# Performance work log

Measured on AMD Instinct MI355X. Metric: run time of the kernel, lower is better.

## Reference

```python
import jax, jax.numpy as jnp
import numpy as np

# dims: B batch, T timesteps, V nodes, D in-features, C channels, d pos-emb dim,
# TS = t_size (spatio-temporal window), P prediction steps, L layers (=4, fixed by GLU(C*4))
B, T, V, D, C, d, TS, P, L = 4, 12, 512, 1, 64, 8, 3, 12, 4
BETA = TS - 1


def setup_inputs() -> dict:
    key = jax.random.key(0)
    ks = jax.random.split(key, 30)
    n = lambda i, shape, s=1.0: jax.random.normal(ks[i], shape, dtype=jnp.float32) * s
    return dict(
        x=n(0, (B, T, V, D)),
        sape=n(1, (V, d)),
        tape=n(2, (B, T, 1, d)),
        srpe=n(3, (V, V, d)),
        trpe=n(4, (TS, 1, d)),
        zeros_x=jnp.zeros((B, BETA, V, C), jnp.float32),
        zeros_tape=jnp.zeros((B, BETA, 1, d), jnp.float32),
        range_mask=(jax.random.uniform(ks[5], (B, V, TS * V)) < 0.5).astype(jnp.float32),
        Wi=n(6, (D, C), D ** -0.5), bi=n(7, (C,), 0.02),
        gc_mu=n(8, (L, 6, d)), gc_sig=n(9, (L, 6, d), 0.5),
        Wg=n(10, (L, C, 2 * C), C ** -0.5), bg=n(11, (L, 2 * C), 0.02),
        Wsp=n(12, (L, d, 2 * C), d ** -0.5), Wtp=n(13, (L, d, 2 * C), d ** -0.5),
        fs_w=n(14, (L, C, C, T), (C * T) ** -0.5), fs_b=n(15, (L, C), 0.02),
        glu1_w=n(16, (L, 2 * C, C), C ** -0.5), glu1_b=n(17, (L, 2 * C), 0.02),
        gout_w=n(18, (8 * C, 4 * C), (4 * C) ** -0.5), gout_b=n(19, (8 * C,), 0.02),
        out_w=n(20, (P, 4 * C), (4 * C) ** -0.5), out_b=n(21, (P,), 0.02),
    )


def _glu_cv(w, b, y):
    # 1x1-conv GLU over channel dim of y: (B, Cin, V) -> (B, Cin, V)
    z = jnp.einsum('oc,bcv->bov', w, y) + b[None, :, None]
    zl, zr = jnp.split(z, 2, axis=1)
    return zl * jax.nn.sigmoid(zr)


def _forward(x, sape, tape, srpe, trpe, Wi, bi, gc_mu, gc_sig, Wg, bg, Wsp, Wtp,
             fs_w, fs_b, glu1_w, glu1_b, gout_w, gout_b, out_w, out_b,
             zeros_x, zeros_tape, range_mask):
    b_, t_ = x.shape[0], x.shape[1]
    v_ = sape.shape[0]
    ts = trpe.shape[0]
    widx = jnp.arange(t_)[:, None] + jnp.arange(ts)  # (T, t_size) sliding-window indices
    h = x @ Wi + bi                                   # InputLayer: B,T,V,C
    tape_pad = jnp.concatenate([zeros_tape, tape], axis=1)  # B,T+beta,1,d
    skips = []
    for l in range(gc_mu.shape[0]):
        mu, sig = gc_mu[l], gc_sig[l]
        gc = lambda emb, i: jnp.sum(-0.5 * (emb - mu[i]) ** 2 * sig[i] ** 2, axis=-1)
        # STPRI: Gaussian position-aware relation inference
        base = gc(sape, 0)[:, None] + gc(sape, 1)[None, :] + gc(srpe, 4)        # (V_i, V_j)
        per_t = gc(tape, 2)[:, :, 0][:, :, None] \
              + gc(tape_pad, 3)[:, :, 0][:, widx] \
              + gc(trpe, 5)[:, 0]                                               # B,T,t_size
        S = jnp.exp(per_t[:, :, :, None, None] + base)                          # B,T,k,i,j (<=1, safe)
        S = S.transpose(0, 1, 4, 2, 3).reshape(b_, t_, v_, ts * v_)             # B,T,j,(k*V+i)
        S = S * range_mask[:, None]                                             # masked relations
        # STPGConv: masked graph conv over the t_size*V window + gating
        x_pad = jnp.concatenate([zeros_x, h], axis=1)                           # B,T+beta,V,C
        xw = x_pad[:, widx].reshape(b_, t_, ts * v_, -1)                        # B,T,t_size*V,C
        g = jnp.einsum('btjm,btmc->btjc', S, xw) @ Wg[l] + bg[l]                # B,T,V,2C
        g = g + sape @ Wsp[l] + tape @ Wtp[l]                                   # +SE(V,2C) +TE(B,T,1,2C)
        gl, gr = jnp.split(g, 2, axis=-1)
        h = gl * jax.nn.sigmoid(gr)                                             # B,T,V,C
        # GFS: conv over time (kernel (1,T)) + GLU -> B,C,V
        y = jnp.einsum('bcvt,oct->bov', h.transpose(0, 3, 2, 1), fs_w[l]) + fs_b[l][None, :, None]
        skips.append(_glu_cv(glu1_w[l], glu1_b[l], y))
    s = _glu_cv(gout_w, gout_b, jnp.concatenate(skips, axis=1))                  # B,4C,V
    return jnp.einsum('oc,bcv->bov', out_w, s) + out_b[None, :, None]            # B,P,V


def reference(x, sape, tape, srpe, trpe, zeros_x, zeros_tape, range_mask, Wi, bi,
              gc_mu, gc_sig, Wg, bg, Wsp, Wtp, fs_w, fs_b, glu1_w, glu1_b,
              gout_w, gout_b, out_w, out_b):
    return _forward(x, sape, tape, srpe, trpe, Wi, bi, gc_mu, gc_sig, Wg, bg, Wsp, Wtp,
                    fs_w, fs_b, glu1_w, glu1_b, gout_w, gout_b, out_w, out_b,
                    zeros_x, zeros_tape, range_mask)
```

## Files before the change

### kernel.cpp

```cpp
#include <hip/hip_runtime.h>
#include <math.h>


typedef unsigned short u16;
typedef __attribute__((ext_vector_type(8))) short short8;
typedef __attribute__((ext_vector_type(4))) float f32x4;
typedef __attribute__((ext_vector_type(8))) unsigned short u16x8;
typedef __attribute__((ext_vector_type(4))) unsigned short u16x4;

#define MFMA16(a, b, c) __builtin_amdgcn_mfma_f32_16x16x32_bf16((a), (b), (c), 0, 0, 0)

__device__ __forceinline__ float b2f(u16 u) {
  union { unsigned int i; float f; } x; x.i = ((unsigned int)u) << 16; return x.f;
}
__device__ __forceinline__ u16 f2b(float f) {
  union { float f; unsigned int i; } x; x.f = f;
  unsigned int r = x.i + 0x7FFFu + ((x.i >> 16) & 1u);
  return (u16)(r >> 16);
}
__device__ __forceinline__ void ld8f(const float* __restrict__ p, float* f) {
  f32x4 a = *(const f32x4*)p;
  f32x4 b = *(const f32x4*)(p + 4);
  #pragma unroll
  for (int i = 0; i < 4; ++i) { f[i] = a[i]; f[4 + i] = b[i]; }
}
__device__ __forceinline__ float gcf(const float* e, const float* __restrict__ mu,
                                     const float* __restrict__ sg) {
  float s = 0.f;
  #pragma unroll
  for (int i = 0; i < 8; ++i) {
    float dm = e[i] - mu[i];
    s += dm * dm * sg[i] * sg[i];
  }
  return -0.5f * s;
}
__device__ __forceinline__ float sigm(float v) { return 1.0f / (1.0f + expf(-v)); }

__global__ __launch_bounds__(256) void prep_kernel(
    const float* __restrict__ x, const float* __restrict__ sape,
    const float* __restrict__ tape, const float* __restrict__ srpe,
    const float* __restrict__ trpe, const float* __restrict__ Wi,
    const float* __restrict__ bi, const float* __restrict__ gmu,
    const float* __restrict__ gsg, const float* __restrict__ Wg,
    const float* __restrict__ bg, const float* __restrict__ Wsp,
    const float* __restrict__ Wtp, const float* __restrict__ fsw,
    const float* __restrict__ mask,
    const float* __restrict__ g1w, const float* __restrict__ gw,
    const float* __restrict__ ow,
    u16* __restrict__ hT0, u16* __restrict__ Abf,
    float* __restrict__ spb, float* __restrict__ tpb,
    u16* __restrict__ fswT, u16* __restrict__ WgT, float* __restrict__ ev,
    u16* __restrict__ g1wB, u16* __restrict__ gwB, u16* __restrict__ owB) {
  const int tid = threadIdx.x;
  int bid = blockIdx.x;

  if (bid < 768) {
    int gid = bid * 256 + tid;
    int i8 = gid & 63, c = (gid >> 6) & 63, bt = gid >> 12;
    float xv[8];
    ld8f(&x[bt * 512 + i8 * 8], xv);
    float wic = Wi[c], bic = bi[c];
    u16x8 hv;
    #pragma unroll
    for (int ii = 0; ii < 8; ++ii) hv[ii] = f2b(xv[ii] * wic + bic);
    *(u16x8*)&hT0[gid * 8] = hv;
    return;
  }
  bid -= 768;
  if (bid < 1024) {
    int gid = bid * 256 + tid;
    int i = gid & 511, j = gid >> 9;
    float fi[8], fj[8], fr[8];
    ld8f(sape + i * 8, fi);
    ld8f(sape + j * 8, fj);
    ld8f(srpe + ((size_t)i * 512 + j) * 8, fr);
    u16 eb[4];
    #pragma unroll
    for (int l = 0; l < 4; ++l) {
      const float* mub = gmu + l * 48;
      const float* sgb = gsg + l * 48;
      float s = gcf(fi, mub + 0, sgb + 0)
              + gcf(fj, mub + 8, sgb + 8)
              + gcf(fr, mub + 32, sgb + 32);
      eb[l] = f2b(expf(s));
    }
    #pragma unroll
    for (int b = 0; b < 4; ++b)
      #pragma unroll
      for (int k = 0; k < 3; ++k) {
        float mv = mask[((size_t)(b * 512 + j)) * 1536 + k * 512 + i];
        u16 m = (mv != 0.f) ? (u16)0xFFFFu : (u16)0;
        #pragma unroll
        for (int l = 0; l < 4; ++l)
          Abf[((size_t)((l * 4 + b) * 512 + j)) * 1536 + k * 512 + i] = eb[l] & m;
      }
    return;
  }
  bid -= 1024;
  if (bid < 1024) {
    int gid = bid * 256 + tid;
    int o = gid & 127, j = (gid >> 7) & 511, l = gid >> 16;
    float s = 0.f;
    #pragma unroll
    for (int dd = 0; dd < 8; ++dd)
      s += sape[j * 8 + dd] * Wsp[(l * 8 + dd) * 128 + o];
    spb[gid] = s;
    return;
  }
  bid -= 1024;
  if (bid < 96) {
    int gid = bid * 256 + tid;
    int o = gid & 127, bt = (gid >> 7) % 48, l = gid / 6144;
    float s = bg[l * 128 + o];
    #pragma unroll
    for (int dd = 0; dd < 8; ++dd)
      s += tape[bt * 8 + dd] * Wtp[(l * 8 + dd) * 128 + o];
    tpb[gid] = s;
    return;
  }
  bid -= 96;
  if (bid < 768) {
    int gid = bid * 256 + tid;
    int kidx = gid % 768, rest = gid / 768;
    int o = rest & 63, l = rest >> 6;
    int c = kidx & 63, tt = kidx >> 6;
    fswT[gid] = f2b(fsw[((l * 64 + o) * 64 + c) * 12 + tt]);
    return;
  }
  bid -= 768;
  if (bid < 128) {
    int gid = bid * 256 + tid;
    int c = gid & 63, o = (gid >> 6) & 127, l = gid >> 13;
    WgT[gid] = f2b(Wg[(l * 64 + c) * 128 + o]);
    return;
  }
  bid -= 128;
  if (bid < 3) {
    int gid = bid * 256 + tid;
    if (gid < 576) {
      int k = gid % 3, t = (gid / 3) % 12, b = (gid / 36) % 4, l = gid / 144;
      const float* mub = gmu + l * 48;
      const float* sgb = gsg + l * 48;
      float e2[8], e3[8], e5[8];
      ld8f(tape + (b * 12 + t) * 8, e2);
      int tp = t + k - 2;
      if (tp >= 0) ld8f(tape + (b * 12 + tp) * 8, e3);
      else {
        #pragma unroll
        for (int ii = 0; ii < 8; ++ii) e3[ii] = 0.f;
      }
      ld8f(trpe + k * 8, e5);
      float s = gcf(e2, mub + 16, sgb + 16)
              + gcf(e3, mub + 24, sgb + 24)
              + gcf(e5, mub + 40, sgb + 40);
      ev[gid] = expf(s);
    }
    return;
  }
  bid -= 3;
  if (bid < 128) {
    int gid = bid * 256 + tid;
    g1wB[gid] = f2b(g1w[gid]);
    return;
  }
  bid -= 128;
  if (bid < 512) {
    int gid = bid * 256 + tid;
    gwB[gid] = f2b(gw[gid]);
    return;
  }
  bid -= 512;
  {
    int gid = bid * 256 + tid;
    if (gid < 3072) owB[gid] = f2b(ow[gid]);
  }
}

__global__ __launch_bounds__(256) void agg_kernel(
    const u16* __restrict__ Abfl, const u16* __restrict__ hT,
    u16* __restrict__ G) {
  __shared__ u16 As[128][72];
  __shared__ u16 Bs[128][72];
  const int tid = threadIdx.x, wid = tid >> 6, lane = tid & 63;
  const int l16 = lane & 15, quad = lane >> 4;
  const int bid = blockIdx.x;
  const int nt = bid / 48;
  const int rest = bid % 48;
  const int mt = rest & 3;
  const int k  = (rest >> 2) % 3;
  const int b  = rest / 12;
  const int wm = wid >> 1, wn = wid & 1;

  const u16* Arow0 = Abfl + ((size_t)(b * 512 + mt * 128)) * 1536 + k * 512;
  f32x4 acc[4][4] = {};

  for (int it = 0; it < 8; ++it) {
    const int i0 = it * 64;
    #pragma unroll
    for (int s = 0; s < 4; ++s) {
      int idx = s * 256 + tid;
      int r = idx >> 3, ch = (idx & 7) * 8;
      *(u16x8*)&As[r][ch] = *(const u16x8*)&Arow0[(size_t)r * 1536 + i0 + ch];
      int tp = nt * 2 + (r >> 6), c = r & 63;
      *(u16x8*)&Bs[r][ch] =
          *(const u16x8*)&hT[((size_t)((b * 12 + tp) * 64 + c)) * 512 + i0 + ch];
    }
    __syncthreads();
    #pragma unroll
    for (int ks = 0; ks < 2; ++ks) {
      short8 af[4], bf[4];
      #pragma unroll
      for (int mb = 0; mb < 4; ++mb)
        af[mb] = *(const short8*)&As[wm * 64 + mb * 16 + l16][ks * 32 + quad * 8];
      #pragma unroll
      for (int nb = 0; nb < 4; ++nb)
        bf[nb] = *(const short8*)&Bs[wn * 64 + nb * 16 + l16][ks * 32 + quad * 8];
      #pragma unroll
      for (int mb = 0; mb < 4; ++mb)
        #pragma unroll
        for (int nb = 0; nb < 4; ++nb)
          acc[mb][nb] = MFMA16(af[mb], bf[nb], acc[mb][nb]);
    }
    __syncthreads();
  }

  u16* base = &As[0][0];
  #pragma unroll
  for (int mb = 0; mb < 4; ++mb)
    #pragma unroll
    for (int nb = 0; nb < 4; ++nb) {
      int n = wn * 64 + nb * 16 + l16;
      #pragma unroll
      for (int r = 0; r < 4; ++r) {
        int m = wm * 64 + mb * 16 + quad * 4 + r;
        base[m * 128 + n] = f2b(acc[mb][nb][r]);
      }
    }
  __syncthreads();
  u16* Gp = G + ((size_t)((b * 3 + k) * 512 + mt * 128)) * 768 + nt * 128;
  #pragma unroll
  for (int s = 0; s < 8; ++s) {
    int idx = s * 256 + tid;
    int m = idx >> 4, ch = (idx & 15) * 8;
    *(u16x8*)&Gp[(size_t)m * 768 + ch] = *(const u16x8*)&base[m * 128 + ch];
  }
}

__global__ __launch_bounds__(256) void combine_kernel(
    const u16* __restrict__ G, const float* __restrict__ evl,
    const u16* __restrict__ WgTl, const float* __restrict__ spbl,
    const float* __restrict__ tpbl, const u16* __restrict__ fswTl,
    u16* __restrict__ hTout, u16* __restrict__ yptl) {
  __shared__ u16 aggL[128][72];
  __shared__ u16 hL[128][72];
  const int tid = threadIdx.x, wid = tid >> 6, lane = tid & 63;
  const int l16 = lane & 15, quad = lane >> 4;
  const int bid = blockIdx.x;
  const int mt = bid & 3;
  const int bt = bid >> 2;
  const int b = bt / 12, t = bt - b * 12;

  {
    int j = tid >> 1;
    int c0 = (tid & 1) * 32;
    float accv[32];
    #pragma unroll
    for (int ii = 0; ii < 32; ++ii) accv[ii] = 0.f;
    #pragma unroll
    for (int k = 0; k < 3; ++k) {
      int tp = t + k - 2;
      if (tp < 0) continue;
      float ek = evl[bt * 3 + k];
      const u16* gp = &G[((size_t)((b * 3 + k) * 512 + mt * 128 + j)) * 768 + tp * 64 + c0];
      #pragma unroll
      for (int s = 0; s < 4; ++s) {
        u16x8 gv = *(const u16x8*)&gp[s * 8];
        #pragma unroll
        for (int ii = 0; ii < 8; ++ii) accv[s * 8 + ii] += b2f(gv[ii]) * ek;
      }
    }
    #pragma unroll
    for (int s = 0; s < 4; ++s) {
      u16x8 ov;
      #pragma unroll
      for (int ii = 0; ii < 8; ++ii) ov[ii] = f2b(accv[s * 8 + ii]);
      *(u16x8*)&aggL[j][c0 + s * 8] = ov;
    }
  }
  __syncthreads();

  f32x4 acc2[8][2] = {};
  #pragma unroll
  for (int ks = 0; ks < 2; ++ks) {
    short8 bf[2];
    #pragma unroll
    for (int nb = 0; nb < 2; ++nb)
      bf[nb] = *(const short8*)&aggL[wid * 32 + nb * 16 + l16][ks * 32 + quad * 8];
    #pragma unroll
    for (int mb = 0; mb < 8; ++mb) {
      short8 a = *(const short8*)&WgTl[(mb * 16 + l16) * 64 + ks * 32 + quad * 8];
      acc2[mb][0] = MFMA16(a, bf[0], acc2[mb][0]);
      acc2[mb][1] = MFMA16(a, bf[1], acc2[mb][1]);
    }
  }

  #pragma unroll
  for (int mb = 0; mb < 4; ++mb) {
    int ob = mb * 16 + quad * 4;
    #pragma unroll
    for (int nb = 0; nb < 2; ++nb) {
      int jl = wid * 32 + nb * 16 + l16;
      int jg = mt * 128 + jl;
      f32x4 spl = *(const f32x4*)&spbl[jg * 128 + ob];
      f32x4 spr = *(const f32x4*)&spbl[jg * 128 + 64 + ob];
      f32x4 tpl = *(const f32x4*)&tpbl[bt * 128 + ob];
      f32x4 tpr = *(const f32x4*)&tpbl[bt * 128 + 64 + ob];
      #pragma unroll
      for (int r = 0; r < 4; ++r) {
        float vl = acc2[mb][nb][r] + spl[r] + tpl[r];
        float vr = acc2[mb + 4][nb][r] + spr[r] + tpr[r];
        u16 hb = f2b(vl * sigm(vr));
        hTout[((size_t)((b * 12 + t) * 64 + ob + r)) * 512 + jg] = hb;
        hL[jl][ob + r] = hb;
      }
    }
  }
  __syncthreads();

  f32x4 accY[4][2] = {};
  #pragma unroll
  for (int ks = 0; ks < 2; ++ks) {
    short8 bfv[2];
    #pragma unroll
    for (int nb = 0; nb < 2; ++nb)
      bfv[nb] = *(const short8*)&hL[wid * 32 + nb * 16 + l16][ks * 32 + quad * 8];
    #pragma unroll
    for (int mb = 0; mb < 4; ++mb) {
      short8 a = *(const short8*)&fswTl[(mb * 16 + l16) * 768 + t * 64 + ks * 32 + quad * 8];
      accY[mb][0] = MFMA16(a, bfv[0], accY[mb][0]);
      accY[mb][1] = MFMA16(a, bfv[1], accY[mb][1]);
    }
  }
  #pragma unroll
  for (int mb = 0; mb < 4; ++mb)
    #pragma unroll
    for (int nb = 0; nb < 2; ++nb) {
      int j = mt * 128 + wid * 32 + nb * 16 + l16;
      #pragma unroll
      for (int r = 0; r < 4; ++r) {
        int o = mb * 16 + quad * 4 + r;
        yptl[((size_t)(bt * 64 + o)) * 512 + j] = f2b(accY[mb][nb][r]);
      }
    }
}

__global__ __launch_bounds__(256) void reduce_kernel(
    const u16* __restrict__ ypt, const float* __restrict__ fsb,
    u16* __restrict__ yB) {
  int gid = blockIdx.x * 256 + threadIdx.x;
  int j4 = gid & 127, o = (gid >> 7) & 63, b = (gid >> 13) & 3, l = gid >> 15;
  const u16* base = &ypt[(size_t)l * 1572864 +
                         ((size_t)((b * 12) * 64 + o)) * 512 + j4 * 4];
  float fb = fsb[l * 64 + o];
  f32x4 s = {fb, fb, fb, fb};
  #pragma unroll
  for (int t = 0; t < 12; ++t) {
    u16x4 v = *(const u16x4*)&base[(size_t)t * 32768];
    #pragma unroll
    for (int ii = 0; ii < 4; ++ii) s[ii] += b2f(v[ii]);
  }
  u16x4 pk;
  #pragma unroll
  for (int ii = 0; ii < 4; ++ii) pk[ii] = f2b(s[ii]);
  *(u16x4*)&yB[((size_t)((l * 4 + b) * 64 + o)) * 512 + j4 * 4] = pk;
}

__global__ __launch_bounds__(256) void glu1cat_kernel(
    const u16* __restrict__ yB, const u16* __restrict__ g1wB,
    const float* __restrict__ g1b, u16* __restrict__ catB) {
  __shared__ u16 yL[128][72];
  const int tid = threadIdx.x, wid = tid >> 6, lane = tid & 63;
  const int l16 = lane & 15, quad = lane >> 4;
  const int l = blockIdx.x >> 4;
  const int b = (blockIdx.x >> 2) & 3;
  const int v0 = (blockIdx.x & 3) * 128;

  {
    int o = tid & 63, sv = tid >> 6;
    const u16* src = &yB[((size_t)((l * 4 + b) * 64 + o)) * 512 + v0 + sv * 32];
    u16x8 p0 = *(const u16x8*)&src[0];
    u16x8 p1 = *(const u16x8*)&src[8];
    u16x8 p2 = *(const u16x8*)&src[16];
    u16x8 p3 = *(const u16x8*)&src[24];
    #pragma unroll
    for (int ii = 0; ii < 8; ++ii) {
      yL[sv * 32 + ii][o] = p0[ii];
      yL[sv * 32 + 8 + ii][o] = p1[ii];
      yL[sv * 32 + 16 + ii][o] = p2[ii];
      yL[sv * 32 + 24 + ii][o] = p3[ii];
    }
  }
  __syncthreads();

  f32x4 acc[2][8] = {};
  #pragma unroll
  for (int ks = 0; ks < 2; ++ks) {
    short8 a0 = *(const short8*)&g1wB[l * 8192 + (wid * 16 + l16) * 64 +
                                      ks * 32 + quad * 8];
    short8 a1 = *(const short8*)&g1wB[l * 8192 + (64 + wid * 16 + l16) * 64 +
                                      ks * 32 + quad * 8];
    #pragma unroll
    for (int nb = 0; nb < 8; ++nb) {
      short8 bf = *(const short8*)&yL[nb * 16 + l16][ks * 32 + quad * 8];
      acc[0][nb] = MFMA16(a0, bf, acc[0][nb]);
      acc[1][nb] = MFMA16(a1, bf, acc[1][nb]);
    }
  }
  #pragma unroll
  for (int nb = 0; nb < 8; ++nb) {
    int v = v0 + nb * 16 + l16;
    int oc = wid * 16 + quad * 4;
    u16x4 pk;
    #pragma unroll
    for (int r = 0; r < 4; ++r) {
      float zl = acc[0][nb][r] + g1b[l * 128 + oc + r];
      float zr = acc[1][nb][r] + g1b[l * 128 + 64 + oc + r];
      pk[r] = f2b(zl * sigm(zr));
    }
    *(u16x4*)&catB[((size_t)(b * 512 + v)) * 256 + l * 64 + oc] = pk;
  }
}

__global__ __launch_bounds__(256) void gout_kernel(
    const u16* __restrict__ catB, const u16* __restrict__ gwB,
    const float* __restrict__ gb, u16* __restrict__ sB) {
  __shared__ u16 cL[64][264];
  const int tid = threadIdx.x, wid = tid >> 6, lane = tid & 63;
  const int l16 = lane & 15, quad = lane >> 4;
  const int wm = wid >> 1, wn = wid & 1;
  const int b = blockIdx.x >> 6;
  const int v0 = ((blockIdx.x >> 3) & 7) * 64;
  const int cc0 = (blockIdx.x & 7) * 32;

  {
    int v = tid >> 2, seg = (tid & 3) * 64;
    const u16* src = &catB[((size_t)(b * 512 + v0 + v)) * 256 + seg];
    #pragma unroll
    for (int s = 0; s < 8; ++s)
      *(u16x8*)&cL[v][seg + s * 8] = *(const u16x8*)&src[s * 8];
  }
  __syncthreads();

  f32x4 acc[2][2] = {};
  #pragma unroll
  for (int ks = 0; ks < 8; ++ks) {
    short8 aL = *(const short8*)&gwB[(cc0 + wm * 16 + l16) * 256 +
                                     ks * 32 + quad * 8];
    short8 aH = *(const short8*)&gwB[(256 + cc0 + wm * 16 + l16) * 256 +
                                     ks * 32 + quad * 8];
    #pragma unroll
    for (int nb = 0; nb < 2; ++nb) {
      short8 bf = *(const short8*)&cL[wn * 32 + nb * 16 + l16][ks * 32 + quad * 8];
      acc[0][nb] = MFMA16(aL, bf, acc[0][nb]);
      acc[1][nb] = MFMA16(aH, bf, acc[1][nb]);
    }
  }
  #pragma unroll
  for (int nb = 0; nb < 2; ++nb) {
    int v = v0 + wn * 32 + nb * 16 + l16;
    int cc = cc0 + wm * 16 + quad * 4;
    u16x4 pk;
    #pragma unroll
    for (int r = 0; r < 4; ++r) {
      float zl = acc[0][nb][r] + gb[cc + r];
      float zr = acc[1][nb][r] + gb[256 + cc + r];
      pk[r] = f2b(zl * sigm(zr));
    }
    *(u16x4*)&sB[((size_t)(b * 512 + v)) * 256 + cc] = pk;
  }
}

__global__ __launch_bounds__(256) void head_kernel(
    const u16* __restrict__ sB, const u16* __restrict__ owB,
    const float* __restrict__ obv, float* __restrict__ out) {
  const int tid = threadIdx.x, wid = tid >> 6, lane = tid & 63;
  const int l16 = lane & 15, quad = lane >> 4;
  const int b = blockIdx.x >> 3;
  const int v0 = (blockIdx.x & 7) * 64;

  f32x4 acc = {};
  #pragma unroll
  for (int ks = 0; ks < 8; ++ks) {
    short8 a;
    if (l16 < 12) a = *(const short8*)&owB[l16 * 256 + ks * 32 + quad * 8];
    else {
      #pragma unroll
      for (int ii = 0; ii < 8; ++ii) a[ii] = 0;
    }
    short8 bf = *(const short8*)&sB[((size_t)(b * 512 + v0 + wid * 16 + l16)) * 256 +
                                    ks * 32 + quad * 8];
    acc = MFMA16(a, bf, acc);
  }
  #pragma unroll
  for (int r = 0; r < 4; ++r) {
    int p = quad * 4 + r;
    if (p < 12)
      out[(b * 12 + p) * 512 + v0 + wid * 16 + l16] = acc[r] + obv[p];
  }
}

extern "C" void kernel_launch(void* const* d_in, const int* in_sizes, int n_in,
                              void* d_out, int out_size, void* d_ws, size_t ws_size,
                              hipStream_t stream) {
  const float* x    = (const float*)d_in[0];
  const float* sape = (const float*)d_in[1];
  const float* tape = (const float*)d_in[2];
  const float* srpe = (const float*)d_in[3];
  const float* trpe = (const float*)d_in[4];
  const float* mask = (const float*)d_in[7];
  const float* Wi   = (const float*)d_in[8];
  const float* bi   = (const float*)d_in[9];
  const float* gmu  = (const float*)d_in[10];
  const float* gsg  = (const float*)d_in[11];
  const float* Wg   = (const float*)d_in[12];
  const float* bg   = (const float*)d_in[13];
  const float* Wsp  = (const float*)d_in[14];
  const float* Wtp  = (const float*)d_in[15];
  const float* fsw  = (const float*)d_in[16];
  const float* fsb  = (const float*)d_in[17];
  const float* g1w  = (const float*)d_in[18];
  const float* g1b  = (const float*)d_in[19];
  const float* gow  = (const float*)d_in[20];
  const float* gob  = (const float*)d_in[21];
  const float* ow   = (const float*)d_in[22];
  const float* obv  = (const float*)d_in[23];

  char* w = (char*)d_ws;
  u16*   hT_a = (u16*)(w + 0);
  u16*   hT_b = (u16*)(w + 3145728);
  u16*   Abf  = (u16*)(w + 6291456);
  u16*   G    = (u16*)(w + 31457280);
  u16*   fswT = (u16*)(w + 40894464);
  u16*   WgT  = (u16*)(w + 41287680);
  u16*   g1wB = (u16*)(w + 41353216);
  u16*   gwB  = (u16*)(w + 41418752);
  u16*   owB  = (u16*)(w + 41680896);
  float* spb  = (float*)(w + 41689088);
  float* tpb  = (float*)(w + 42737664);
  float* ev   = (float*)(w + 42835968);
  u16*   ypt  = (u16*)(w + 42852352);
  u16*   yB   = (u16*)(w + 55435264);
  u16*   catB = (u16*)(w + 57532416);
  u16*   sB   = (u16*)(w + 58580992);

  prep_kernel<<<4463, 256, 0, stream>>>(x, sape, tape, srpe, trpe, Wi, bi, gmu, gsg,
                                        Wg, bg, Wsp, Wtp, fsw, mask, g1w, gow, ow,
                                        hT_a, Abf, spb, tpb, fswT, WgT, ev,
                                        g1wB, gwB, owB);
  u16* hin = hT_a;
  u16* hout = hT_b;
  for (int l = 0; l < 4; ++l) {
    agg_kernel<<<288, 256, 0, stream>>>(Abf + (size_t)l * 3145728, hin, G);
    combine_kernel<<<192, 256, 0, stream>>>(G, ev + l * 144, WgT + l * 8192,
                                            spb + l * 65536, tpb + l * 6144,
                                            fswT + l * 49152, hout,
                                            ypt + (size_t)l * 1572864);
    u16* tmp = hin; hin = hout; hout = tmp;
  }
  reduce_kernel<<<512, 256, 0, stream>>>(ypt, fsb, yB);
  glu1cat_kernel<<<64, 256, 0, stream>>>(yB, g1wB, g1b, catB);
  gout_kernel<<<256, 256, 0, stream>>>(catB, gwB, gob, sB);
  head_kernel<<<32, 256, 0, stream>>>(sB, owB, obv, (float*)d_out);
}
```

Baseline: 237.1 us.

## Fuse time reduction into glu1cat and remap agg blocks for XCD locality

The separate reduce kernel that summed the per-timestep GFS partials is removed. Its work now happens inside glu1cat, which accumulates the 12 timesteps in registers before writing to shared memory. This drops one launch and the yB intermediate round trip, but concentrates the reduction reads in only 64 blocks. Separately, agg_kernel's block index is remapped so blocks with the same batch share an XCD (bid&7), aiming to improve L2 reuse of the A operand.

New measurement: 245.9 us. 1.04x slower.

```diff
diff --git a/kernel.cpp b/kernel.cpp
--- a/kernel.cpp
+++ b/kernel.cpp
@@ -184,11 +184,15 @@
   const int tid = threadIdx.x, wid = tid >> 6, lane = tid & 63;
   const int l16 = lane & 15, quad = lane >> 4;
   const int bid = blockIdx.x;
-  const int nt = bid / 48;
-  const int rest = bid % 48;
-  const int mt = rest & 3;
-  const int k  = (rest >> 2) % 3;
-  const int b  = rest / 12;
+  const int xcd = bid & 7;
+  const int b   = xcd >> 1;
+  const int ntg = xcd & 1;
+  const int rest = bid >> 3;
+  const int ntr = rest % 3;
+  const int km  = rest / 3;
+  const int mt  = km & 3;
+  const int k   = km >> 2;
+  const int nt  = ntg * 3 + ntr;
   const int wm = wid >> 1, wn = wid & 1;
 
   const u16* Arow0 = Abfl + ((size_t)(b * 512 + mt * 128)) * 1536 + k * 512;
@@ -354,30 +358,10 @@
     }
 }
 
-__global__ __launch_bounds__(256) void reduce_kernel(
+__global__ __launch_bounds__(256) void glu1cat_kernel(
     const u16* __restrict__ ypt, const float* __restrict__ fsb,
-    u16* __restrict__ yB) {
-  int gid = blockIdx.x * 256 + threadIdx.x;
-  int j4 = gid & 127, o = (gid >> 7) & 63, b = (gid >> 13) & 3, l = gid >> 15;
-  const u16* base = &ypt[(size_t)l * 1572864 +
-                         ((size_t)((b * 12) * 64 + o)) * 512 + j4 * 4];
-  float fb = fsb[l * 64 + o];
-  f32x4 s = {fb, fb, fb, fb};
-  #pragma unroll
-  for (int t = 0; t < 12; ++t) {
-    u16x4 v = *(const u16x4*)&base[(size_t)t * 32768];
-    #pragma unroll
-    for (int ii = 0; ii < 4; ++ii) s[ii] += b2f(v[ii]);
-  }
-  u16x4 pk;
-  #pragma unroll
-  for (int ii = 0; ii < 4; ++ii) pk[ii] = f2b(s[ii]);
-  *(u16x4*)&yB[((size_t)((l * 4 + b) * 64 + o)) * 512 + j4 * 4] = pk;
-}
-
-__global__ __launch_bounds__(256) void glu1cat_kernel(
-    const u16* __restrict__ yB, const u16* __restrict__ g1wB,
-    const float* __restrict__ g1b, u16* __restrict__ catB) {
+    const u16* __restrict__ g1wB, const float* __restrict__ g1b,
+    u16* __restrict__ catB) {
   __shared__ u16 yL[128][72];
   const int tid = threadIdx.x, wid = tid >> 6, lane = tid & 63;
   const int l16 = lane & 15, quad = lane >> 4;
@@ -387,18 +371,22 @@
 
   {
     int o = tid & 63, sv = tid >> 6;
-    const u16* src = &yB[((size_t)((l * 4 + b) * 64 + o)) * 512 + v0 + sv * 32];
-    u16x8 p0 = *(const u16x8*)&src[0];
-    u16x8 p1 = *(const u16x8*)&src[8];
-    u16x8 p2 = *(const u16x8*)&src[16];
-    u16x8 p3 = *(const u16x8*)&src[24];
-    #pragma unroll
-    for (int ii = 0; ii < 8; ++ii) {
-      yL[sv * 32 + ii][o] = p0[ii];
-      yL[sv * 32 + 8 + ii][o] = p1[ii];
-      yL[sv * 32 + 16 + ii][o] = p2[ii];
-      yL[sv * 32 + 24 + ii][o] = p3[ii];
-    }
+    float accv[32];
+    float fb = fsb[l * 64 + o];
+    #pragma unroll
+    for (int ii = 0; ii < 32; ++ii) accv[ii] = fb;
+    for (int t = 0; t < 12; ++t) {
+      const u16* src = &ypt[(size_t)l * 1572864 +
+                            ((size_t)((b * 12 + t) * 64 + o)) * 512 + v0 + sv * 32];
+      #pragma unroll
+      for (int s = 0; s < 4; ++s) {
+        u16x8 v = *(const u16x8*)&src[s * 8];
+        #pragma unroll
+        for (int ii = 0; ii < 8; ++ii) accv[s * 8 + ii] += b2f(v[ii]);
+      }
+    }
+    #pragma unroll
+    for (int ii = 0; ii < 32; ++ii) yL[sv * 32 + ii][o] = f2b(accv[ii]);
   }
   __syncthreads();
 
@@ -549,9 +537,8 @@
   float* tpb  = (float*)(w + 42737664);
   float* ev   = (float*)(w + 42835968);
   u16*   ypt  = (u16*)(w + 42852352);
-  u16*   yB   = (u16*)(w + 55435264);
-  u16*   catB = (u16*)(w + 57532416);
-  u16*   sB   = (u16*)(w + 58580992);
+  u16*   catB = (u16*)(w + 55435264);
+  u16*   sB   = (u16*)(w + 56483840);
 
   prep_kernel<<<4463, 256, 0, stream>>>(x, sape, tape, srpe, trpe, Wi, bi, gmu, gsg,
                                         Wg, bg, Wsp, Wtp, fsw, mask, g1w, gow, ow,
@@ -567,8 +554,7 @@
                                             ypt + (size_t)l * 1572864);
     u16* tmp = hin; hin = hout; hout = tmp;
   }
-  reduce_kernel<<<512, 256, 0, stream>>>(ypt, fsb, yB);
-  glu1cat_kernel<<<64, 256, 0, stream>>>(yB, g1wB, g1b, catB);
+  glu1cat_kernel<<<64, 256, 0, stream>>>(ypt, fsb, g1wB, g1b, catB);
   gout_kernel<<<256, 256, 0, stream>>>(catB, gwB, gob, sB);
   head_kernel<<<32, 256, 0, stream>>>(sB, owB, obv, (float*)d_out);
 }
```
